# Performance work log

Hardware: AMD Instinct MI355X
Metric: run time of the kernel (lower is better)

Reference implementation:

```python
import jax, jax.numpy as jnp
import numpy as np

N = 8192       # num nodes
D_IN = 256     # in_features
D_OUT = 128    # out_features per head
H = 2          # num_heads
E = 262144     # num edges (avg degree 32)
ALPHA = 0.2    # leaky relu slope


def setup_inputs() -> dict:
    key = jax.random.key(0)
    k1, k2, k3, k4 = jax.random.split(key, 4)
    x = jax.random.normal(k1, (N, D_IN), dtype=jnp.float32)
    # per-head Linear weights: W[h] is [out, in] (y = x @ W.T), a[h] is [2*out]
    W = jax.random.normal(k2, (H, D_OUT, D_IN), dtype=jnp.float32) * (1.0 / np.sqrt(D_IN))
    a = jax.random.normal(k3, (H, 2 * D_OUT), dtype=jnp.float32) * (1.0 / np.sqrt(2 * D_OUT))
    edge_index = jax.random.randint(k4, (2, E), 0, N, dtype=jnp.int32)
    return {"x": x, "W": W, "a": a, "edge_index": edge_index}


def reference(x, W, a, edge_index):
    # h[h,n,d] = W(x) per head
    h = jnp.einsum('nf,hdf->hnd', x, W)
    # a([h_i ; h_j]) decomposes into a_src . h_i + a_dst . h_j
    a_src, a_dst = a[:, :D_OUT], a[:, D_OUT:]
    s_i = jnp.einsum('hnd,hd->hn', h, a_src)
    s_j = jnpp_dummy = None
    s_j = jnp.einsum('hnd,hd->hn', h, a_dst)
    score = s_i[:, :, None] + s_j[:, None, :]  # [H, n, n]
    # dense adjacency mask from edge list
    adj = jnp.zeros((N, N), dtype=jnp.bool_).at[edge_index[0], edge_index[1]].set(True)
    # faithful to original: non-edges set to 0 (NOT -inf) before leaky_relu + softmax
    e = jnp.where(adj[None, :, :], score, jnp.float32(0.0))
    e = jnp.where(e > 0, e, ALPHA * e)  # leaky relu
    att = jax.nn.softmax(e, axis=-1)    # softmax over j (dim=1 of original [n,n])
    out = jnp.einsum('hij,hjd->hid', att, h)  # aggregate: attention @ h
    out = jnp.transpose(out, (1, 0, 2)).reshape(N, H * D_OUT)  # concat heads
    return jax.nn.elu(out)
```

## Files before the change

### kernel.cpp

```cpp
#include <hip/hip_runtime.h>
#include <hip/hip_bf16.h>

#define N_NODES 8192
#define DIN     256
#define DOUT    128
#define NHEAD   2
#define CTOT    256
#define NWORDS  256
#define LRELU_A 0.2f
#define CAPN    128
#define LDR     40

typedef __attribute__((ext_vector_type(8))) short bf16x8;
typedef __attribute__((ext_vector_type(4))) float f32x4;

__device__ __forceinline__ float bf(unsigned short u) {
    return __uint_as_float((unsigned)u << 16);
}
__device__ __forceinline__ unsigned short f2bf(float f) {
    unsigned u = __float_as_uint(f);
    u = (u + 0x7fffu + ((u >> 16) & 1u)) >> 16;
    return (unsigned short)u;
}
__device__ __forceinline__ unsigned pk(float a, float b) {
    return (unsigned)f2bf(a) | ((unsigned)f2bf(b) << 16);
}

__global__ __launch_bounds__(256) void k_pre(const float* __restrict__ x,
                                             const float* __restrict__ W,
                                             const float* __restrict__ a,
                                             unsigned short* __restrict__ hb16,
                                             float* __restrict__ sp_src,
                                             float* __restrict__ sp_dst,
                                             float4* __restrict__ adjp,
                                             float4* __restrict__ sallp) {
    __shared__ unsigned short As[64 * LDR];
    __shared__ unsigned short Bs[64 * LDR];
    int b = blockIdx.x, t = threadIdx.x;

    if (b == 2560) {
        if (t < 64) sallp[t] = make_float4(0.f, 0.f, 0.f, 0.f);
        return;
    }
    if (b >= 512) {
        adjp[(b - 512) * 256 + t] = make_float4(0.f, 0.f, 0.f, 0.f);
        return;
    }

    int bm = (b & 127) * 64;
    int bn = (b >> 7) * 64;
    int wv = t >> 6, lane = t & 63;
    int fr = lane & 15, ksl = lane >> 4;

    f32x4 acc[4] = {};
    for (int k0 = 0; k0 < DIN; k0 += 32) {
        {
            int row = t >> 2, slot = t & 3;
            const float4* srcA = reinterpret_cast<const float4*>(&x[(bm + row) * DIN + k0 + slot * 8]);
            float4 va0 = srcA[0], va1 = srcA[1];
            *reinterpret_cast<uint4*>(&As[row * LDR + slot * 8]) =
                make_uint4(pk(va0.x, va0.y), pk(va0.z, va0.w), pk(va1.x, va1.y), pk(va1.z, va1.w));
            const float4* srcB = reinterpret_cast<const float4*>(&W[(bn + row) * DIN + k0 + slot * 8]);
            float4 vb0 = srcB[0], vb1 = srcB[1];
            *reinterpret_cast<uint4*>(&Bs[row * LDR + slot * 8]) =
                make_uint4(pk(vb0.x, vb0.y), pk(vb0.z, vb0.w), pk(vb1.x, vb1.y), pk(vb1.z, vb1.w));
        }
        __syncthreads();
        bf16x8 af = *reinterpret_cast<const bf16x8*>(&As[(wv * 16 + fr) * LDR + ksl * 8]);
        #pragma unroll
        for (int fn = 0; fn < 4; ++fn) {
            bf16x8 bfr = *reinterpret_cast<const bf16x8*>(&Bs[(fn * 16 + fr) * LDR + ksl * 8]);
            acc[fn] = __builtin_amdgcn_mfma_f32_16x16x32_bf16(af, bfr, acc[fn], 0, 0, 0);
        }
        __syncthreads();
    }

    #pragma unroll
    for (int fn = 0; fn < 4; ++fn) {
        int c = bn + fn * 16 + fr;
        int r0 = bm + wv * 16 + ksl * 4;
        #pragma unroll
        for (int r = 0; r < 4; ++r)
            hb16[(size_t)(r0 + r) * CTOT + c] = f2bf(acc[fn][r]);
    }

    int head = (bn >= 128);
    int q    = bn >> 6;
    float as[4], ad[4];
    #pragma unroll
    for (int fn = 0; fn < 4; ++fn) {
        int d = (bn & 127) + fn * 16 + fr;
        as[fn] = a[head * 256 + d];
        ad[fn] = a[head * 256 + 128 + d];
    }
    #pragma unroll
    for (int r = 0; r < 4; ++r) {
        float ps = acc[0][r] * as[0] + acc[1][r] * as[1] + acc[2][r] * as[2] + acc[3][r] * as[3];
        float pd = acc[0][r] * ad[0] + acc[1][r] * ad[1] + acc[2][r] * ad[2] + acc[3][r] * ad[3];
        #pragma unroll
        for (int off = 8; off; off >>= 1) {
            ps += __shfl_xor(ps, off);
            pd += __shfl_xor(pd, off);
        }
        if (fr == 0) {
            int row = bm + wv * 16 + ksl * 4 + r;
            sp_src[q * N_NODES + row] = ps;
            sp_dst[q * N_NODES + row] = pd;
        }
    }
}

__global__ __launch_bounds__(256) void k_mid(const int* __restrict__ ei, int E,
                                             unsigned int* __restrict__ adjw,
                                             const float* __restrict__ sp_src,
                                             const float* __restrict__ sp_dst,
                                             const unsigned short* __restrict__ hb16,
                                             float* __restrict__ s_src,
                                             float* __restrict__ s_dst,
                                             float* __restrict__ S_all) {
    int b = blockIdx.x, t = threadIdx.x;

    if (b < 1024) {
        int e = b * 256 + t;
        if (e < E) {
            int src = ei[e];
            int dst = ei[E + e];
            atomicOr(&adjw[(size_t)src * NWORDS + (dst >> 5)], 1u << (dst & 31));
        }
        return;
    }
    if (b < 1056) {
        int n = (b - 1024) * 256 + t;
        s_src[n]           = sp_src[0 * N_NODES + n] + sp_src[1 * N_NODES + n];
        s_src[N_NODES + n] = sp_src[2 * N_NODES + n] + sp_src[3 * N_NODES + n];
        s_dst[n]           = sp_dst[0 * N_NODES + n] + sp_dst[1 * N_NODES + n];
        s_dst[N_NODES + n] = sp_dst[2 * N_NODES + n] + sp_dst[3 * N_NODES + n];
        return;
    }

    int r0 = (b - 1056) * 16;
    float s = 0.f;
    #pragma unroll
    for (int r = r0; r < r0 + 16; ++r)
        s += bf(hb16[r * CTOT + t]);
    atomicAdd(&S_all[t], s);
}

__global__ __launch_bounds__(256) void k_attn(const unsigned int* __restrict__ adjw,
                                              const float* __restrict__ s_src,
                                              const float* __restrict__ s_dst,
                                              const unsigned short* __restrict__ hb16,
                                              const float* __restrict__ S_all,
                                              float* __restrict__ out) {
    __shared__ unsigned short nbr[4][CAPN];
    __shared__ float          ewl[4][CAPN];

    int i    = blockIdx.x;
    int t    = threadIdx.x;
    int wv   = t >> 6;
    int lane = t & 63;
    int head = wv >> 1;
    int c    = wv * 64 + lane;

    const uint4 wq = reinterpret_cast<const uint4*>(adjw + (size_t)i * NWORDS)[lane];
    int cnt = __popc(wq.x) + __popc(wq.y) + __popc(wq.z) + __popc(wq.w);
    int inc = cnt;
    #pragma unroll
    for (int off = 1; off < 64; off <<= 1) {
        int v = __shfl_up(inc, off);
        if (lane >= off) inc += v;
    }
    int deg = __shfl(inc, 63);
    int pos = inc - cnt;
    int idb = lane * 128;
    {
        unsigned int w;
        w = wq.x; while (w) { int bb = __ffs(w) - 1; w &= w - 1; if (pos < CAPN) nbr[wv][pos] = (unsigned short)(idb + bb);      ++pos; }
        w = wq.y; while (w) { int bb = __ffs(w) - 1; w &= w - 1; if (pos < CAPN) nbr[wv][pos] = (unsigned short)(idb + 32 + bb); ++pos; }
        w = wq.z; while (w) { int bb = __ffs(w) - 1; w &= w - 1; if (pos < CAPN) nbr[wv][pos] = (unsigned short)(idb + 64 + bb); ++pos; }
        w = wq.w; while (w) { int bb = __ffs(w) - 1; w &= w - 1; if (pos < CAPN) nbr[wv][pos] = (unsigned short)(idb + 96 + bb); ++pos; }
    }
    if (deg > CAPN) deg = CAPN;

    float ssh = s_src[head * N_NODES + i];
    const float* sdh = s_dst + head * N_NODES;
    float z = 0.f;
    for (int k = lane; k < deg; k += 64) {
        int j = nbr[wv][k];
        float v = ssh + sdh[j];
        float e = v > 0.f ? v : LRELU_A * v;
        float w = expf(e) - 1.f;
        ewl[wv][k] = w;
        z += w;
    }
    #pragma unroll
    for (int off = 32; off; off >>= 1)
        z += __shfl_xor(z, off);
    float Z = (float)N_NODES + z;

    float acc = 0.f;
    int k = 0;
    for (; k + 8 <= deg; k += 8) {
        int j0 = nbr[wv][k+0], j1 = nbr[wv][k+1], j2 = nbr[wv][k+2], j3 = nbr[wv][k+3];
        int j4 = nbr[wv][k+4], j5 = nbr[wv][k+5], j6 = nbr[wv][k+6], j7 = nbr[wv][k+7];
        float w0 = ewl[wv][k+0], w1 = ewl[wv][k+1], w2 = ewl[wv][k+2], w3 = ewl[wv][k+3];
        float w4 = ewl[wv][k+4], w5 = ewl[wv][k+5], w6 = ewl[wv][k+6], w7 = ewl[wv][k+7];
        float v0 = bf(hb16[j0 * CTOT + c]);
        float v1 = bf(hb16[j1 * CTOT + c]);
        float v2 = bf(hb16[j2 * CTOT + c]);
        float v3 = bf(hb16[j3 * CTOT + c]);
        float v4 = bf(hb16[j4 * CTOT + c]);
        float v5 = bf(hb16[j5 * CTOT + c]);
        float v6 = bf(hb16[j6 * CTOT + c]);
        float v7 = bf(hb16[j7 * CTOT + c]);
        acc = fmaf(w0, v0, acc); acc = fmaf(w1, v1, acc);
        acc = fmaf(w2, v2, acc); acc = fmaf(w3, v3, acc);
        acc = fmaf(w4, v4, acc); acc = fmaf(w5, v5, acc);
        acc = fmaf(w6, v6, acc); acc = fmaf(w7, v7, acc);
    }
    for (; k + 4 <= deg; k += 4) {
        int j0 = nbr[wv][k], j1 = nbr[wv][k+1], j2 = nbr[wv][k+2], j3 = nbr[wv][k+3];
        float w0 = ewl[wv][k], w1 = ewl[wv][k+1], w2 = ewl[wv][k+2], w3 = ewl[wv][k+3];
        float v0 = bf(hb16[j0 * CTOT + c]);
        float v1 = bf(hb16[j1 * CTOT + c]);
        float v2 = bf(hb16[j2 * CTOT + c]);
        float v3 = bf(hb16[j3 * CTOT + c]);
        acc = fmaf(w0, v0, acc); acc = fmaf(w1, v1, acc);
        acc = fmaf(w2, v2, acc); acc = fmaf(w3, v3, acc);
    }
    for (; k < deg; ++k)
        acc = fmaf(ewl[wv][k], bf(hb16[nbr[wv][k] * CTOT + c]), acc);

    float o = (S_all[c] + acc) / Z;
    o = o > 0.f ? o : expm1f(o);
    out[i * CTOT + c] = o;
}

extern "C" void kernel_launch(void* const* d_in, const int* in_sizes, int n_in,
                              void* d_out, int out_size, void* d_ws, size_t ws_size,
                              hipStream_t stream) {
    const float* x  = (const float*)d_in[0];
    const float* W  = (const float*)d_in[1];
    const float* a  = (const float*)d_in[2];
    const int*   ei = (const int*)d_in[3];
    int E = in_sizes[3] / 2;
    float* out = (float*)d_out;

    char* ws = (char*)d_ws;
    size_t off = 0;
    auto alloc = [&](size_t bytes) { char* p = ws + off; off += (bytes + 255) & ~(size_t)255; return p; };
    unsigned int*   adjw   = (unsigned int*)  alloc((size_t)N_NODES * NWORDS * 4);
    float*          S_all  = (float*)         alloc(CTOT * 4);
    float*          s_src  = (float*)         alloc((size_t)NHEAD * N_NODES * 4);
    float*          s_dst  = (float*)         alloc((size_t)NHEAD * N_NODES * 4);
    unsigned short* hb16   = (unsigned short*)alloc((size_t)N_NODES * CTOT * 2);
    float*          sp_src = (float*)         alloc((size_t)4 * N_NODES * 4);
    float*          sp_dst = (float*)         alloc((size_t)4 * N_NODES * 4);

    k_pre<<<2561, 256, 0, stream>>>(x, W, a, hb16, sp_src, sp_dst, (float4*)adjw, (float4*)S_all);
    k_mid<<<1568, 256, 0, stream>>>(ei, E, adjw, sp_src, sp_dst, hb16, s_src, s_dst, S_all);
    k_attn<<<N_NODES, 256, 0, stream>>>(adjw, s_src, s_dst, hb16, S_all, out);
}
```

Measured before the change: 67.43 us.

## Load full K into swizzled LDS for GEMM; split neighbor gather across waves

The projection GEMM now stages the whole 256-wide K dimension of x and W tiles into XOR-swizzled LDS once and runs the MFMA loop without a barrier per K step. The attention kernel changes from one column per lane, with each wave walking every neighbor, to each wave handling a strided quarter of the neighbors over the full 256-column row. It loads 8-byte bf16 chunks (4 columns per lane) and reduces the partial sums across waves in LDS before a vectorized float4 epilogue. The aim is fewer GEMM synchronisations and wider, more coalesced gather loads. The cost is more LDS per block (64 KB) and an extra cross-wave reduction with one more barrier.

```diff
diff --git a/kernel.cpp b/kernel.cpp
--- a/kernel.cpp
+++ b/kernel.cpp
@@ -9,7 +9,6 @@
 #define NWORDS  256
 #define LRELU_A 0.2f
 #define CAPN    128
-#define LDR     40
 
 typedef __attribute__((ext_vector_type(8))) short bf16x8;
 typedef __attribute__((ext_vector_type(4))) float f32x4;
@@ -17,6 +16,8 @@
 __device__ __forceinline__ float bf(unsigned short u) {
     return __uint_as_float((unsigned)u << 16);
 }
+__device__ __forceinline__ float bflo(unsigned u) { return __uint_as_float(u << 16); }
+__device__ __forceinline__ float bfhi(unsigned u) { return __uint_as_float(u & 0xffff0000u); }
 __device__ __forceinline__ unsigned short f2bf(float f) {
     unsigned u = __float_as_uint(f);
     u = (u + 0x7fffu + ((u >> 16) & 1u)) >> 16;
@@ -34,8 +35,8 @@
                                              float* __restrict__ sp_dst,
                                              float4* __restrict__ adjp,
                                              float4* __restrict__ sallp) {
-    __shared__ unsigned short As[64 * LDR];
-    __shared__ unsigned short Bs[64 * LDR];
+    __shared__ unsigned short As[64 * 256];
+    __shared__ unsigned short Bs[64 * 256];
     int b = blockIdx.x, t = threadIdx.x;
 
     if (b == 2560) {
@@ -52,27 +53,40 @@
     int wv = t >> 6, lane = t & 63;
     int fr = lane & 15, ksl = lane >> 4;
 
+    #pragma unroll
+    for (int i = 0; i < 16; ++i) {
+        int idx = i * 256 + t;
+        int row = idx >> 6;
+        int kq  = (idx & 63) * 4;
+        float4 v = *reinterpret_cast<const float4*>(&x[(bm + row) * DIN + kq]);
+        int slot = kq >> 3, half = (kq >> 2) & 1;
+        *reinterpret_cast<uint2*>(&As[row * 256 + ((slot ^ (row & 7)) << 3) + half * 4]) =
+            make_uint2(pk(v.x, v.y), pk(v.z, v.w));
+    }
+    #pragma unroll
+    for (int i = 0; i < 16; ++i) {
+        int idx = i * 256 + t;
+        int row = idx >> 6;
+        int kq  = (idx & 63) * 4;
+        float4 v = *reinterpret_cast<const float4*>(&W[(bn + row) * DIN + kq]);
+        int slot = kq >> 3, half = (kq >> 2) & 1;
+        *reinterpret_cast<uint2*>(&Bs[row * 256 + ((slot ^ (row & 7)) << 3) + half * 4]) =
+            make_uint2(pk(v.x, v.y), pk(v.z, v.w));
+    }
+    __syncthreads();
+
     f32x4 acc[4] = {};
-    for (int k0 = 0; k0 < DIN; k0 += 32) {
-        {
-            int row = t >> 2, slot = t & 3;
-            const float4* srcA = reinterpret_cast<const float4*>(&x[(bm + row) * DIN + k0 + slot * 8]);
-            float4 va0 = srcA[0], va1 = srcA[1];
-            *reinterpret_cast<uint4*>(&As[row * LDR + slot * 8]) =
-                make_uint4(pk(va0.x, va0.y), pk(va0.z, va0.w), pk(va1.x, va1.y), pk(va1.z, va1.w));
-            const float4* srcB = reinterpret_cast<const float4*>(&W[(bn + row) * DIN + k0 + slot * 8]);
-            float4 vb0 = srcB[0], vb1 = srcB[1];
-            *reinterpret_cast<uint4*>(&Bs[row * LDR + slot * 8]) =
-                make_uint4(pk(vb0.x, vb0.y), pk(vb0.z, vb0.w), pk(vb1.x, vb1.y), pk(vb1.z, vb1.w));
-        }
-        __syncthreads();
-        bf16x8 af = *reinterpret_cast<const bf16x8*>(&As[(wv * 16 + fr) * LDR + ksl * 8]);
+    #pragma unroll
+    for (int ch = 0; ch < 8; ++ch) {
+        int s = ch * 4 + ksl;
+        int ra = wv * 16 + fr;
+        bf16x8 af = *reinterpret_cast<const bf16x8*>(&As[ra * 256 + ((s ^ (ra & 7)) << 3)]);
         #pragma unroll
         for (int fn = 0; fn < 4; ++fn) {
-            bf16x8 bfr = *reinterpret_cast<const bf16x8*>(&Bs[(fn * 16 + fr) * LDR + ksl * 8]);
+            int rb = fn * 16 + fr;
+            bf16x8 bfr = *reinterpret_cast<const bf16x8*>(&Bs[rb * 256 + ((s ^ (rb & 7)) << 3)]);
             acc[fn] = __builtin_amdgcn_mfma_f32_16x16x32_bf16(af, bfr, acc[fn], 0, 0, 0);
         }
-        __syncthreads();
     }
 
     #pragma unroll
@@ -154,13 +168,14 @@
                                               float* __restrict__ out) {
     __shared__ unsigned short nbr[4][CAPN];
     __shared__ float          ewl[4][CAPN];
+    __shared__ float          zr[4];
+    __shared__ float4         part[4][64];
 
     int i    = blockIdx.x;
     int t    = threadIdx.x;
     int wv   = t >> 6;
     int lane = t & 63;
     int head = wv >> 1;
-    int c    = wv * 64 + lane;
 
     const uint4 wq = reinterpret_cast<const uint4*>(adjw + (size_t)i * NWORDS)[lane];
     int cnt = __popc(wq.x) + __popc(wq.y) + __popc(wq.z) + __popc(wq.w);
@@ -196,44 +211,60 @@
     #pragma unroll
     for (int off = 32; off; off >>= 1)
         z += __shfl_xor(z, off);
-    float Z = (float)N_NODES + z;
-
-    float acc = 0.f;
-    int k = 0;
-    for (; k + 8 <= deg; k += 8) {
-        int j0 = nbr[wv][k+0], j1 = nbr[wv][k+1], j2 = nbr[wv][k+2], j3 = nbr[wv][k+3];
-        int j4 = nbr[wv][k+4], j5 = nbr[wv][k+5], j6 = nbr[wv][k+6], j7 = nbr[wv][k+7];
-        float w0 = ewl[wv][k+0], w1 = ewl[wv][k+1], w2 = ewl[wv][k+2], w3 = ewl[wv][k+3];
-        float w4 = ewl[wv][k+4], w5 = ewl[wv][k+5], w6 = ewl[wv][k+6], w7 = ewl[wv][k+7];
-        float v0 = bf(hb16[j0 * CTOT + c]);
-        float v1 = bf(hb16[j1 * CTOT + c]);
-        float v2 = bf(hb16[j2 * CTOT + c]);
-        float v3 = bf(hb16[j3 * CTOT + c]);
-        float v4 = bf(hb16[j4 * CTOT + c]);
-        float v5 = bf(hb16[j5 * CTOT + c]);
-        float v6 = bf(hb16[j6 * CTOT + c]);
-        float v7 = bf(hb16[j7 * CTOT + c]);
-        acc = fmaf(w0, v0, acc); acc = fmaf(w1, v1, acc);
-        acc = fmaf(w2, v2, acc); acc = fmaf(w3, v3, acc);
-        acc = fmaf(w4, v4, acc); acc = fmaf(w5, v5, acc);
-        acc = fmaf(w6, v6, acc); acc = fmaf(w7, v7, acc);
-    }
-    for (; k + 4 <= deg; k += 4) {
-        int j0 = nbr[wv][k], j1 = nbr[wv][k+1], j2 = nbr[wv][k+2], j3 = nbr[wv][k+3];
-        float w0 = ewl[wv][k], w1 = ewl[wv][k+1], w2 = ewl[wv][k+2], w3 = ewl[wv][k+3];
-        float v0 = bf(hb16[j0 * CTOT + c]);
-        float v1 = bf(hb16[j1 * CTOT + c]);
-        float v2 = bf(hb16[j2 * CTOT + c]);
-        float v3 = bf(hb16[j3 * CTOT + c]);
-        acc = fmaf(w0, v0, acc); acc = fmaf(w1, v1, acc);
-        acc = fmaf(w2, v2, acc); acc = fmaf(w3, v3, acc);
-    }
-    for (; k < deg; ++k)
-        acc = fmaf(ewl[wv][k], bf(hb16[nbr[wv][k] * CTOT + c]), acc);
-
-    float o = (S_all[c] + acc) / Z;
-    o = o > 0.f ? o : expm1f(o);
-    out[i * CTOT + c] = o;
+    if (lane == 0) zr[wv] = (float)N_NODES + z;
+    __syncthreads();
+
+    const uint2* hb2 = reinterpret_cast<const uint2*>(hb16);
+    bool lo = lane < 32;
+    float4 acc = make_float4(0.f, 0.f, 0.f, 0.f);
+    int k = wv;
+    for (; k + 28 < deg; k += 32) {
+        int   jj[8]; float ww[8]; uint2 hv[8];
+        #pragma unroll
+        for (int u = 0; u < 8; ++u) {
+            int kk = k + u * 4;
+            jj[u] = nbr[wv][kk];
+            ww[u] = lo ? ewl[0][kk] : ewl[2][kk];
+            hv[u] = hb2[jj[u] * 64 + lane];
+        }
+        #pragma unroll
+        for (int u = 0; u < 8; ++u) {
+            acc.x = fmaf(ww[u], bflo(hv[u].x), acc.x);
+            acc.y = fmaf(ww[u], bfhi(hv[u].x), acc.y);
+            acc.z = fmaf(ww[u], bflo(hv[u].y), acc.z);
+            acc.w = fmaf(ww[u], bfhi(hv[u].y), acc.w);
+        }
+    }
+    for (; k < deg; k += 4) {
+        int j = nbr[wv][k];
+        float w = lo ? ewl[0][k] : ewl[2][k];
+        uint2 hv = hb2[j * 64 + lane];
+        acc.x = fmaf(w, bflo(hv.x), acc.x);
+        acc.y = fmaf(w, bfhi(hv.x), acc.y);
+        acc.z = fmaf(w, bflo(hv.y), acc.z);
+        acc.w = fmaf(w, bfhi(hv.y), acc.w);
+    }
+    part[wv][lane] = acc;
+    __syncthreads();
+
+    if (t < 64) {
+        float4 c0 = part[0][t], c1 = part[1][t], c2 = part[2][t], c3 = part[3][t];
+        float4 s;
+        s.x = c0.x + c1.x + c2.x + c3.x;
+        s.y = c0.y + c1.y + c2.y + c3.y;
+        s.z = c0.z + c1.z + c2.z + c3.z;
+        s.w = c0.w + c1.w + c2.w + c3.w;
+        float4 sa = reinterpret_cast<const float4*>(S_all)[t];
+        float rz = 1.f / ((t >= 32) ? zr[2] : zr[0]);
+        float4 o;
+        o.x = (sa.x + s.x) * rz; o.y = (sa.y + s.y) * rz;
+        o.z = (sa.z + s.z) * rz; o.w = (sa.w + s.w) * rz;
+        o.x = o.x > 0.f ? o.x : expm1f(o.x);
+        o.y = o.y > 0.f ? o.y : expm1f(o.y);
+        o.z = o.z > 0.f ? o.z : expm1f(o.z);
+        o.w = o.w > 0.f ? o.w : expm1f(o.w);
+        reinterpret_cast<float4*>(out)[i * 64 + t] = o;
+    }
 }
 
 extern "C" void kernel_launch(void* const* d_in, const int* in_sizes, int n_in,
```

Result: faster. 64.12 us (-4.9%).
